# Performance work log

Measured on AMD Instinct MI355X. Metric: run time of the kernel, lower is better.

## Reference

```python
import jax, jax.numpy as jnp
import numpy as np

N, E = 50000, 1250000
IN_DIM, H, C, EDGE_DIM = 128, 2, 32, 64
NEG_SLOPE = 0.2


def setup_inputs() -> dict:
    key = jax.random.key(0)
    ks = jax.random.split(key, 9)
    x = jax.random.normal(ks[0], (N, IN_DIM), dtype=jnp.float32)
    edge_index = jax.random.randint(ks[1], (2, E), 0, N, dtype=jnp.int64)
    edge_attr = jax.random.normal(ks[2], (E, EDGE_DIM), dtype=jnp.float32)
    # learned params (PyG GATConv: glorot-style scale)
    W = jax.random.normal(ks[3], (IN_DIM, H * C), dtype=jnp.float32) * (1.0 / np.sqrt(IN_DIM))
    W_edge = jax.random.normal(ks[4], (EDGE_DIM, H * C), dtype=jnp.float32) * (1.0 / np.sqrt(EDGE_DIM))
    att_src = jax.random.normal(ks[5], (H, C), dtype=jnp.float32) * (1.0 / np.sqrt(C))
    att_dst = jax.random.normal(ks[6], (H, C), dtype=jnp.float32) * (1.0 / np.sqrt(C))
    att_edge = jax.random.normal(ks[7], (H, C), dtype=jnp.float32) * (1.0 / np.sqrt(C))
    bias = jnp.zeros((H * C,), dtype=jnp.float32)
    return {"x": x, "edge_index": edge_index, "edge_attr": edge_attr,
            "W": W, "W_edge": W_edge, "att_src": att_src, "att_dst": att_dst,
            "att_edge": att_edge, "bias": bias}


def reference(x, edge_index, edge_attr, W, W_edge, att_src, att_dst, att_edge, bias):
    # IntraGraphAttention.forward: relu then GATConv(in, 32, heads=2, edge_dim=64)
    x = jax.nn.relu(x)
    src, dst = edge_index[0], edge_index[1]

    # PyG add_self_loops(fill_value='mean'): self-loop edge_attr = mean of
    # incoming edge attrs per node (zeros for isolated nodes).
    deg = jax.ops.segment_sum(jnp.ones((E,), jnp.float32), dst, num_segments=N)
    loop_attr = jax.ops.segment_sum(edge_attr, dst, num_segments=N) / jnp.maximum(deg, 1.0)[:, None]
    loop_idx = jnp.arange(N, dtype=src.dtype)
    src_f = jnp.concatenate([src, loop_idx])          # [E+N]
    dst_f = jnp.concatenate([dst, loop_idx])          # [E+N]
    eattr_f = jnp.concatenate([edge_attr, loop_attr])  # [E+N, 64]

    # node / edge projections
    h = (x @ W).reshape(N, H, C)                       # [N,H,C]
    a_src = jnp.einsum('nhc,hc->nh', h, att_src)       # [N,H]
    a_dst = jnp.einsum('nhc,hc->nh', h, att_dst)       # [N,H]
    e = (eattr_f @ W_edge).reshape(-1, H, C)           # [E+N,H,C]
    a_edge = jnp.einsum('ehc,hc->eh', e, att_edge)     # [E+N,H]

    # per-edge attention logits
    alpha = a_src[src_f] + a_dst[dst_f] + a_edge       # [E+N,H]
    alpha = jax.nn.leaky_relu(alpha, NEG_SLOPE)

    # segment softmax over destination neighborhoods
    amax = jax.ops.segment_max(alpha, dst_f, num_segments=N)  # [N,H]
    p = jnp.exp(alpha - amax[dst_f])
    denom = jax.ops.segment_sum(p, dst_f, num_segments=N)     # [N,H]
    alpha = p / (denom[dst_f] + 1e-16)

    # scatter-aggregate messages (dropout dp=0 -> identity)
    msg = h[src_f] * alpha[..., None]                   # [E+N,H,C]
    out = jax.ops.segment_sum(msg, dst_f, num_segments=N)     # [N,H,C]
    return out.reshape(N, H * C) + bias
```

## Files before the change

kernel.cpp:

```cpp
#include <hip/hip_runtime.h>

#define NEG 0.2f

__global__ __launch_bounds__(256) void k_zero(int* __restrict__ p, int n) {
    int i = blockIdx.x * 256 + threadIdx.x;
    if (i < n) p[i] = 0;
}

__global__ __launch_bounds__(128) void k_node(
    const float* __restrict__ x, const float* __restrict__ W,
    const float* __restrict__ att_src, const float* __restrict__ att_dst,
    float* __restrict__ hbuf, float* __restrict__ a_src, float* __restrict__ a_dst, int N) {
    __shared__ float xs[128 * 36];
    __shared__ float Wl[128 * 64];
    const int t  = threadIdx.x;
    const int tn = t & 7;
    const int tc = t >> 3;
    const int node0 = blockIdx.x * 32;

    for (int j = t; j < 128 * 64; j += 128) Wl[j] = W[j];
    for (int j = t; j < 32 * 128; j += 128) {
        int n = j >> 7, k = j & 127;
        int nn = node0 + n;
        xs[k * 36 + n] = (nn < N) ? fmaxf(x[(size_t)nn * 128 + k], 0.f) : 0.f;
    }
    __syncthreads();

    float4 acc[4] = {{0,0,0,0},{0,0,0,0},{0,0,0,0},{0,0,0,0}};
#pragma unroll 8
    for (int k = 0; k < 128; ++k) {
        const float4 xv = *(const float4*)(xs + k * 36 + 4 * tn);
        const float4 wv = *(const float4*)(Wl + k * 64 + 4 * tc);
        acc[0].x = fmaf(xv.x, wv.x, acc[0].x); acc[0].y = fmaf(xv.x, wv.y, acc[0].y);
        acc[0].z = fmaf(xv.x, wv.z, acc[0].z); acc[0].w = fmaf(xv.x, wv.w, acc[0].w);
        acc[1].x = fmaf(xv.y, wv.x, acc[1].x); acc[1].y = fmaf(xv.y, wv.y, acc[1].y);
        acc[1].z = fmaf(xv.y, wv.z, acc[1].z); acc[1].w = fmaf(xv.y, wv.w, acc[1].w);
        acc[2].x = fmaf(xv.z, wv.x, acc[2].x); acc[2].y = fmaf(xv.z, wv.y, acc[2].y);
        acc[2].z = fmaf(xv.z, wv.z, acc[2].z); acc[2].w = fmaf(xv.z, wv.w, acc[2].w);
        acc[3].x = fmaf(xv.w, wv.x, acc[3].x); acc[3].y = fmaf(xv.w, wv.y, acc[3].y);
        acc[3].z = fmaf(xv.w, wv.z, acc[3].z); acc[3].w = fmaf(xv.w, wv.w, acc[3].w);
    }

#pragma unroll
    for (int n = 0; n < 4; ++n) {
        int nn = node0 + 4 * tn + n;
        if (nn < N) *(float4*)(hbuf + (size_t)nn * 64 + 4 * tc) = acc[n];
    }

    const float4 as4 = *(const float4*)(att_src + 4 * tc);
    const float4 ad4 = *(const float4*)(att_dst + 4 * tc);
    int head = (t >= 64) ? 1 : 0;
#pragma unroll
    for (int n = 0; n < 4; ++n) {
        float vs = acc[n].x * as4.x + acc[n].y * as4.y + acc[n].z * as4.z + acc[n].w * as4.w;
        float vd = acc[n].x * ad4.x + acc[n].y * ad4.y + acc[n].z * ad4.z + acc[n].w * ad4.w;
#pragma unroll
        for (int m = 8; m <= 32; m <<= 1) {
            vs += __shfl_xor(vs, m, 64);
            vd += __shfl_xor(vd, m, 64);
        }
        int nn = node0 + 4 * tn + n;
        if ((t & 63) < 8 && nn < N) {
            a_src[nn * 2 + head] = vs;
            a_dst[nn * 2 + head] = vd;
        }
    }
}

__global__ __launch_bounds__(256) void k_hist(
    const int* __restrict__ dstI, int* __restrict__ count, long long E,
    const float* __restrict__ W_edge, const float* __restrict__ att_edge,
    float* __restrict__ wke) {
    if (blockIdx.x == 0 && threadIdx.x < 128) {
        int hh = threadIdx.x >> 6;
        int k  = threadIdx.x & 63;
        float s = 0.f;
#pragma unroll
        for (int c = 0; c < 32; ++c)
            s += W_edge[k * 64 + hh * 32 + c] * att_edge[hh * 32 + c];
        wke[hh * 64 + k] = s;
    }
    long long i0 = (long long)blockIdx.x * 256 + threadIdx.x;
    long long stride = (long long)gridDim.x * 256;
    for (long long i = i0; i < E; i += stride)
        atomicAdd(&count[dstI[i]], 1);
}

__global__ __launch_bounds__(256) void k_scan1(const int* __restrict__ cnt, int* __restrict__ offs,
                                               int* __restrict__ bsum, int N) {
    __shared__ int ts[256];
    int t = threadIdx.x, blk = blockIdx.x;
    int base = blk * 1024 + t * 4;
    int v[4], s = 0;
#pragma unroll
    for (int i = 0; i < 4; ++i) {
        int idx = base + i;
        v[i] = (idx < N) ? cnt[idx] : 0;
        s += v[i];
    }
    ts[t] = s;
    __syncthreads();
    for (int off = 1; off < 256; off <<= 1) {
        int y = (t >= off) ? ts[t - off] : 0;
        __syncthreads();
        ts[t] += y;
        __syncthreads();
    }
    int run = ts[t] - s;
#pragma unroll
    for (int i = 0; i < 4; ++i) {
        int idx = base + i;
        if (idx < N) offs[idx] = run;
        run += v[i];
    }
    if (t == 255) bsum[blk] = ts[255];
}

__global__ void k_scan2(int* __restrict__ bsum, int nb) {
    int t = threadIdx.x;
    int orig = (t < nb) ? bsum[t] : 0;
    int v = orig;
#pragma unroll
    for (int off = 1; off < 64; off <<= 1) {
        int y = __shfl_up(v, off, 64);
        if (t >= off) v += y;
    }
    if (t < nb) bsum[t] = v - orig;
}

__global__ void k_scan3(int* __restrict__ offs, const int* __restrict__ bsum,
                        int* __restrict__ cursor, int N) {
    int idx = blockIdx.x * 256 + threadIdx.x;
    if (idx < N) {
        int o = offs[idx] + bsum[idx >> 10];
        offs[idx] = o;
        cursor[idx] = o;
    }
}

__global__ __launch_bounds__(256) void k_sort(
    const int* __restrict__ srcI, const int* __restrict__ dstI,
    int* __restrict__ cursor, int2* __restrict__ epos, long long E) {
    long long i0 = (long long)blockIdx.x * 256 + threadIdx.x;
    long long stride = (long long)gridDim.x * 256;
    for (long long e = i0; e < E; e += stride) {
        int s = srcI[e], d = dstI[e];
        int pos = atomicAdd(&cursor[d], 1);
        epos[pos] = make_int2((int)e, s);
    }
}

__global__ __launch_bounds__(256) void k_agg(
    const int2* __restrict__ epos, const int* __restrict__ offs,
    const int* __restrict__ count, const float* __restrict__ edge_attr,
    const float* __restrict__ wke, const float* __restrict__ a_src,
    const float* __restrict__ a_dst, const float* __restrict__ hbuf,
    const float* __restrict__ bias, float* __restrict__ out, int N) {
    __shared__ float wkes[128];
    int t = threadIdx.x;
    if (t < 128) wkes[t] = wke[t];
    __syncthreads();
    int lane = t & 63;
    int sub = lane & 15;
    int grp = lane >> 4;
    int n = blockIdx.x * 4 + (t >> 6);
    if (n >= N) return;
    int cnt  = count[n];
    int base = offs[n];
    const float4 wa = *(const float4*)(wkes + sub * 4);
    const float4 wb = *(const float4*)(wkes + 64 + sub * 4);
    float ad0 = a_dst[n * 2 + 0], ad1 = a_dst[n * 2 + 1];
    float accx = 0.f, accy = 0.f, accz = 0.f, accw = 0.f;
    float den0 = 0.f, den1 = 0.f, sae0 = 0.f, sae1 = 0.f;

    if (cnt > 0) {
        int last = cnt - 1;
        int2 epA = epos[base + (grp < cnt ? grp : last)];
        int2 epB = epos[base + (grp + 4 < cnt ? grp + 4 : last)];
        float4 eaA = *(const float4*)(edge_attr + (size_t)epA.x * 64 + sub * 4);
        float2 asA = *(const float2*)(a_src + 2 * (size_t)epA.y);
        float4 hvA = *(const float4*)(hbuf + (size_t)epA.y * 64 + sub * 4);
        for (int j = grp; j < cnt; j += 4) {
            int jc = j + 8 < cnt ? j + 8 : last;
            int2 epC = epos[base + jc];
            float4 eaB = *(const float4*)(edge_attr + (size_t)epB.x * 64 + sub * 4);
            float2 asB = *(const float2*)(a_src + 2 * (size_t)epB.y);
            float4 hvB = *(const float4*)(hbuf + (size_t)epB.y * 64 + sub * 4);
            float pa0 = eaA.x * wa.x + eaA.y * wa.y + eaA.z * wa.z + eaA.w * wa.w;
            float pa1 = eaA.x * wb.x + eaA.y * wb.y + eaA.z * wb.z + eaA.w * wb.w;
#pragma unroll
            for (int m = 1; m <= 8; m <<= 1) {
                pa0 += __shfl_xor(pa0, m, 64);
                pa1 += __shfl_xor(pa1, m, 64);
            }
            float l0 = asA.x + ad0 + pa0; l0 = l0 > 0.f ? l0 : NEG * l0;
            float l1 = asA.y + ad1 + pa1; l1 = l1 > 0.f ? l1 : NEG * l1;
            float q0 = __expf(l0), q1 = __expf(l1);
            float q = (sub < 8) ? q0 : q1;
            accx = fmaf(q, hvA.x, accx);
            accy = fmaf(q, hvA.y, accy);
            accz = fmaf(q, hvA.z, accz);
            accw = fmaf(q, hvA.w, accw);
            den0 += q0; den1 += q1;
            sae0 += pa0; sae1 += pa1;
            epA = epB; eaA = eaB; asA = asB; hvA = hvB;
            epB = epC;
        }
    }
#define RED2(v) { v += __shfl_xor(v, 16, 64); v += __shfl_xor(v, 32, 64); }
    RED2(accx) RED2(accy) RED2(accz) RED2(accw)
    RED2(den0) RED2(den1) RED2(sae0) RED2(sae1)
#undef RED2

    float dg = (cnt > 0) ? (float)cnt : 1.f;
    float as0 = a_src[n * 2 + 0], as1 = a_src[n * 2 + 1];
    float l0 = as0 + ad0 + sae0 / dg; l0 = l0 > 0.f ? l0 : NEG * l0;
    float l1 = as1 + ad1 + sae1 / dg; l1 = l1 > 0.f ? l1 : NEG * l1;
    float pl0 = __expf(l0), pl1 = __expf(l1);
    const float4 hn = *(const float4*)(hbuf + (size_t)n * 64 + sub * 4);
    float pl  = (sub < 8) ? pl0 : pl1;
    float den = ((sub < 8) ? den0 + pl0 : den1 + pl1) + 1e-16f;
    const float4 bv = *(const float4*)(bias + sub * 4);
    if (grp == 0) {
        float4 o;
        o.x = (accx + pl * hn.x) / den + bv.x;
        o.y = (accy + pl * hn.y) / den + bv.y;
        o.z = (accz + pl * hn.z) / den + bv.z;
        o.w = (accw + pl * hn.w) / den + bv.w;
        *(float4*)(out + (size_t)n * 64 + sub * 4) = o;
    }
}

extern "C" void kernel_launch(void* const* d_in, const int* in_sizes, int n_in,
                              void* d_out, int out_size, void* d_ws, size_t ws_size,
                              hipStream_t stream) {
    const float* x         = (const float*)d_in[0];
    const int*   ei        = (const int*)d_in[1];
    const float* edge_attr = (const float*)d_in[2];
    const float* W         = (const float*)d_in[3];
    const float* W_edge    = (const float*)d_in[4];
    const float* att_src   = (const float*)d_in[5];
    const float* att_dst   = (const float*)d_in[6];
    const float* att_edge  = (const float*)d_in[7];
    const float* bias      = (const float*)d_in[8];

    int N = in_sizes[0] / 128;
    long long E = in_sizes[1] / 2;
    const int* srcI = ei;
    const int* dstI = ei + E;

    char* ws = (char*)d_ws;
    int2*  epos   = (int2*)ws;                        ws += (size_t)E * 8;
    float* wke    = (float*)ws;                       ws += 128 * 4;
    float* hbuf   = (float*)ws;                       ws += (size_t)N * 64 * 4;
    float* a_src  = (float*)ws;                       ws += (size_t)N * 2 * 4;
    float* a_dst  = (float*)ws;                       ws += (size_t)N * 2 * 4;
    int*   count  = (int*)ws;                         ws += (size_t)N * 4;
    int*   offs   = (int*)ws;                         ws += (size_t)N * 4;
    int*   cursor = (int*)ws;                         ws += (size_t)N * 4;
    int*   bsum   = (int*)ws;                         ws += 64 * 4;

    k_zero<<<(N + 255) / 256, 256, 0, stream>>>(count, N);
    k_node<<<(N + 31) / 32, 128, 0, stream>>>(x, W, att_src, att_dst, hbuf, a_src, a_dst, N);
    k_hist<<<2048, 256, 0, stream>>>(dstI, count, E, W_edge, att_edge, wke);

    int nb = (N + 1023) / 1024;
    k_scan1<<<nb, 256, 0, stream>>>(count, offs, bsum, N);
    k_scan2<<<1, 64, 0, stream>>>(bsum, nb);
    k_scan3<<<(N + 255) / 256, 256, 0, stream>>>(offs, bsum, cursor, N);

    k_sort<<<2048, 256, 0, stream>>>(srcI, dstI, cursor, epos, E);

    k_agg<<<(N + 3) / 4, 256, 0, stream>>>(epos, offs, count, edge_attr, wke, a_src, a_dst,
                                           hbuf, bias, (float*)d_out, N);
}
```

Before: 334.4 us.

## Precompute per-edge attention logits in a streaming pass before aggregation

Adds a kernel that reads edge_attr sequentially and writes two projected edge logits per edge into a workspace buffer. The aggregation kernel then gathers 8 bytes per edge instead of a 256-byte edge_attr row and drops the shuffle reduction, cutting random-access traffic. The histogram/scan/sort pipeline is now launched twice in a loop, which doubles that work for no apparent reason. The change also needs an extra E*8 bytes of workspace.

```diff
diff --git a/kernel.cpp b/kernel.cpp
--- a/kernel.cpp
+++ b/kernel.cpp
@@ -150,16 +150,36 @@
     }
 }
 
+__global__ __launch_bounds__(256) void k_paseq(
+    const float* __restrict__ edge_attr, const float* __restrict__ wke,
+    float2* __restrict__ pa2, long long E) {
+    __shared__ float wkes[128];
+    if (threadIdx.x < 128) wkes[threadIdx.x] = wke[threadIdx.x];
+    __syncthreads();
+    long long i0 = (long long)blockIdx.x * 256 + threadIdx.x;
+    long long stride = (long long)gridDim.x * 256;
+    for (long long e = i0; e < E; e += stride) {
+        const float4* row = (const float4*)(edge_attr + e * 64);
+        float pa0 = 0.f, pa1 = 0.f;
+#pragma unroll
+        for (int k = 0; k < 16; ++k) {
+            float4 ea = row[k];
+            float4 wa = *(const float4*)(wkes + k * 4);
+            float4 wb = *(const float4*)(wkes + 64 + k * 4);
+            pa0 += ea.x * wa.x + ea.y * wa.y + ea.z * wa.z + ea.w * wa.w;
+            pa1 += ea.x * wb.x + ea.y * wb.y + ea.z * wb.z + ea.w * wb.w;
+        }
+        pa2[e] = make_float2(pa0, pa1);
+    }
+}
+
 __global__ __launch_bounds__(256) void k_agg(
-    const int2* __restrict__ epos, const int* __restrict__ offs,
-    const int* __restrict__ count, const float* __restrict__ edge_attr,
-    const float* __restrict__ wke, const float* __restrict__ a_src,
-    const float* __restrict__ a_dst, const float* __restrict__ hbuf,
-    const float* __restrict__ bias, float* __restrict__ out, int N) {
-    __shared__ float wkes[128];
+    const int2* __restrict__ epos, const float2* __restrict__ pa2,
+    const int* __restrict__ offs, const int* __restrict__ count,
+    const float* __restrict__ a_src, const float* __restrict__ a_dst,
+    const float* __restrict__ hbuf, const float* __restrict__ bias,
+    float* __restrict__ out, int N) {
     int t = threadIdx.x;
-    if (t < 128) wkes[t] = wke[t];
-    __syncthreads();
     int lane = t & 63;
     int sub = lane & 15;
     int grp = lane >> 4;
@@ -167,8 +187,6 @@
     if (n >= N) return;
     int cnt  = count[n];
     int base = offs[n];
-    const float4 wa = *(const float4*)(wkes + sub * 4);
-    const float4 wb = *(const float4*)(wkes + 64 + sub * 4);
     float ad0 = a_dst[n * 2 + 0], ad1 = a_dst[n * 2 + 1];
     float accx = 0.f, accy = 0.f, accz = 0.f, accw = 0.f;
     float den0 = 0.f, den1 = 0.f, sae0 = 0.f, sae1 = 0.f;
@@ -177,24 +195,17 @@
         int last = cnt - 1;
         int2 epA = epos[base + (grp < cnt ? grp : last)];
         int2 epB = epos[base + (grp + 4 < cnt ? grp + 4 : last)];
-        float4 eaA = *(const float4*)(edge_attr + (size_t)epA.x * 64 + sub * 4);
+        float2 paA = pa2[epA.x];
         float2 asA = *(const float2*)(a_src + 2 * (size_t)epA.y);
         float4 hvA = *(const float4*)(hbuf + (size_t)epA.y * 64 + sub * 4);
         for (int j = grp; j < cnt; j += 4) {
             int jc = j + 8 < cnt ? j + 8 : last;
             int2 epC = epos[base + jc];
-            float4 eaB = *(const float4*)(edge_attr + (size_t)epB.x * 64 + sub * 4);
+            float2 paB = pa2[epB.x];
             float2 asB = *(const float2*)(a_src + 2 * (size_t)epB.y);
             float4 hvB = *(const float4*)(hbuf + (size_t)epB.y * 64 + sub * 4);
-            float pa0 = eaA.x * wa.x + eaA.y * wa.y + eaA.z * wa.z + eaA.w * wa.w;
-            float pa1 = eaA.x * wb.x + eaA.y * wb.y + eaA.z * wb.z + eaA.w * wb.w;
-#pragma unroll
-            for (int m = 1; m <= 8; m <<= 1) {
-                pa0 += __shfl_xor(pa0, m, 64);
-                pa1 += __shfl_xor(pa1, m, 64);
-            }
-            float l0 = asA.x + ad0 + pa0; l0 = l0 > 0.f ? l0 : NEG * l0;
-            float l1 = asA.y + ad1 + pa1; l1 = l1 > 0.f ? l1 : NEG * l1;
+            float l0 = asA.x + ad0 + paA.x; l0 = l0 > 0.f ? l0 : NEG * l0;
+            float l1 = asA.y + ad1 + paA.y; l1 = l1 > 0.f ? l1 : NEG * l1;
             float q0 = __expf(l0), q1 = __expf(l1);
             float q = (sub < 8) ? q0 : q1;
             accx = fmaf(q, hvA.x, accx);
@@ -202,8 +213,8 @@
             accz = fmaf(q, hvA.z, accz);
             accw = fmaf(q, hvA.w, accw);
             den0 += q0; den1 += q1;
-            sae0 += pa0; sae1 += pa1;
-            epA = epB; eaA = eaB; asA = asB; hvA = hvB;
+            sae0 += paA.x; sae1 += paA.y;
+            epA = epB; paA = paB; asA = asB; hvA = hvB;
             epB = epC;
         }
     }
@@ -250,27 +261,32 @@
     const int* dstI = ei + E;
 
     char* ws = (char*)d_ws;
-    int2*  epos   = (int2*)ws;                        ws += (size_t)E * 8;
-    float* wke    = (float*)ws;                       ws += 128 * 4;
-    float* hbuf   = (float*)ws;                       ws += (size_t)N * 64 * 4;
-    float* a_src  = (float*)ws;                       ws += (size_t)N * 2 * 4;
-    float* a_dst  = (float*)ws;                       ws += (size_t)N * 2 * 4;
-    int*   count  = (int*)ws;                         ws += (size_t)N * 4;
-    int*   offs   = (int*)ws;                         ws += (size_t)N * 4;
-    int*   cursor = (int*)ws;                         ws += (size_t)N * 4;
-    int*   bsum   = (int*)ws;                         ws += 64 * 4;
-
-    k_zero<<<(N + 255) / 256, 256, 0, stream>>>(count, N);
+    int2*  epos   = (int2*)ws;                 ws += (size_t)E * 8;
+    float2* pa2   = (float2*)ws;               ws += (size_t)E * 8;
+    float* wke    = (float*)ws;                ws += 128 * 4;
+    float* hbuf   = (float*)ws;                ws += (size_t)N * 64 * 4;
+    float* a_src  = (float*)ws;                ws += (size_t)N * 2 * 4;
+    float* a_dst  = (float*)ws;                ws += (size_t)N * 2 * 4;
+    int*   count  = (int*)ws;                  ws += (size_t)N * 4;
+    int*   offs   = (int*)ws;                  ws += (size_t)N * 4;
+    int*   cursor = (int*)ws;                  ws += (size_t)N * 4;
+    int*   bsum   = (int*)ws;                  ws += 64 * 4;
+
+    int nb = (N + 1023) / 1024;
+
     k_node<<<(N + 31) / 32, 128, 0, stream>>>(x, W, att_src, att_dst, hbuf, a_src, a_dst, N);
-    k_hist<<<2048, 256, 0, stream>>>(dstI, count, E, W_edge, att_edge, wke);
-
-    int nb = (N + 1023) / 1024;
-    k_scan1<<<nb, 256, 0, stream>>>(count, offs, bsum, N);
-    k_scan2<<<1, 64, 0, stream>>>(bsum, nb);
-    k_scan3<<<(N + 255) / 256, 256, 0, stream>>>(offs, bsum, cursor, N);
-
-    k_sort<<<2048, 256, 0, stream>>>(srcI, dstI, cursor, epos, E);
-
-    k_agg<<<(N + 3) / 4, 256, 0, stream>>>(epos, offs, count, edge_attr, wke, a_src, a_dst,
-                                           hbuf, bias, (float*)d_out, N);
-}
+
+    for (int rep = 0; rep < 2; ++rep) {
+        k_zero<<<(N + 255) / 256, 256, 0, stream>>>(count, N);
+        k_hist<<<2048, 256, 0, stream>>>(dstI, count, E, W_edge, att_edge, wke);
+        k_scan1<<<nb, 256, 0, stream>>>(count, offs, bsum, N);
+        k_scan2<<<1, 64, 0, stream>>>(bsum, nb);
+        k_scan3<<<(N + 255) / 256, 256, 0, stream>>>(offs, bsum, cursor, N);
+        k_sort<<<2048, 256, 0, stream>>>(srcI, dstI, cursor, epos, E);
+    }
+
+    k_paseq<<<2048, 256, 0, stream>>>(edge_attr, wke, pa2, E);
+
+    k_agg<<<(N + 3) / 4, 256, 0, stream>>>(epos, pa2, offs, count, a_src, a_dst, hbuf,
+                                           bias, (float*)d_out, N);
+}
```

New measurement: 536.2 us. 60.4% more time.
